# Kernel tuning notes

Hardware: AMD Instinct MI355X
Metric: run time of the kernel (lower is better)

The kernel has to match this reference:

```python
import jax, jax.numpy as jnp
import numpy as np

B = 16; L_IN = 512; D_MODEL = 512; N_HEAD = 8; D_K = 128; D_V = 128
D_FF = 2048; N_LAYER = 4; WINDOW = (4, 4, 4); INNER = 5; COV = 4; NUM_SEQ = 128
N_LVL = len(WINDOW) + 1


def _build_mask_sizes():
    # Pyraformer get_mask: intra-scale band + inter-scale parent/child links.
    all_size = [L_IN]
    for w in WINDOW:
        all_size.append(all_size[-1] // w)
    L = sum(all_size)
    vis = np.zeros((L, L), dtype=bool)
    iw = INNER // 2
    starts = [0]
    for s in all_size:
        starts.append(starts[-1] + s)
    for li, sz in enumerate(all_size):
        s = starts[li]
        for i in range(s, s + sz):
            vis[i, max(i - iw, s):min(i + iw + 1, s + sz)] = True
    for li in range(1, len(all_size)):
        s = starts[li]
        for i in range(s, s + all_size[li]):
            l = (s - all_size[li - 1]) + (i - s) * WINDOW[li - 1]
            if i == s + all_size[li] - 1:
                r = s
            else:
                r = (s - all_size[li - 1]) + (i - s + 1) * WINDOW[li - 1]
            vis[i, l:r] = True
            vis[l:r, i] = True
    return ~vis, all_size  # True = blocked


def _build_indexes(all_size):
    # Pyraformer refer_points: for each fine position, its ancestor at each scale.
    idx = np.zeros((L_IN, len(all_size)), dtype=np.int64)
    for i in range(L_IN):
        idx[i, 0] = i
        former = i
        for j in range(1, len(all_size)):
            start = sum(all_size[:j])
            inner = former - (start - all_size[j - 1])
            former = start + min(inner // WINDOW[j - 1], all_size[j] - 1)
            idx[i, j] = former
    return idx


def _layer_norm(x, g, b, eps=1e-5):
    m = x.mean(-1, keepdims=True)
    v = x.var(-1, keepdims=True)
    return (x - m) / jnp.sqrt(v + eps) * g + b


def _conv1d(x, w, stride):  # x: [B,C,L], w: [O,I,K]
    return jax.lax.conv_general_dilated(x, w, (stride,), 'VALID',
                                        dimension_numbers=('NCH', 'OIH', 'NCH'))


def _forward(x, cov_w, cov_b, data_conv_w, down_w, down_b, conv_w, conv_b, bn_g, bn_b,
             up_w, up_b, bln_g, bln_b, wq, wk, wv, fc_w, ln1_g, ln1_b,
             ffn_w1, ffn_b1, ffn_w2, ffn_b2, ln2_g, ln2_b, attn_mask, gather_idx):
    Bsz = x.shape[0]
    # SingleStepEmbedding
    covs = jnp.concatenate([x[:, :, 1:1 + COV], (x[:, :, -1] / NUM_SEQ - 0.5)[..., None]], -1)
    cov_emb = covs @ cov_w + cov_b
    data = x[:, :, 0][:, None, :]                      # [B,1,L]
    data = jnp.concatenate([data[:, :, -1:], data, data[:, :, :1]], -1)  # circular pad k=3
    data_emb = _conv1d(data, data_conv_w, 1).transpose(0, 2, 1)          # [B,L,D]
    i = jnp.arange(D_MODEL)
    vec = jnp.power(10000.0, 2.0 * (i // 2) / D_MODEL)
    ang = jnp.arange(L_IN)[:, None] / vec
    pos_emb = jnp.where(i % 2 == 0, jnp.sin(ang), jnp.cos(ang))
    seq = cov_emb + data_emb + pos_emb[None]
    # Bottleneck_Construct (down -> strided convs -> up -> concat -> LN)
    tmp = (seq @ down_w + down_b).transpose(0, 2, 1)   # [B,d_k,L]
    outs = []
    for s in range(len(WINDOW)):
        tmp = _conv1d(tmp, conv_w[s], WINDOW[s]) + conv_b[s][None, :, None]
        mu = tmp.mean((0, 2), keepdims=True)
        var = tmp.var((0, 2), keepdims=True)
        tmp = (tmp - mu) / jnp.sqrt(var + 1e-5) * bn_g[s][None, :, None] + bn_b[s][None, :, None]
        tmp = jax.nn.elu(tmp)
        outs.append(tmp)
    pyr = jnp.concatenate(outs, axis=2).transpose(0, 2, 1) @ up_w + up_b
    enc = _layer_norm(jnp.concatenate([seq, pyr], axis=1), bln_g, bln_b)  # [B,Ltot,D]
    Lt = enc.shape[1]
    scale = np.float32(1.0 / np.sqrt(D_K))
    for l in range(N_LAYER):
        q = (enc @ wq[l]).reshape(Bsz, Lt, N_HEAD, D_K).transpose(0, 2, 1, 3)
        k = (enc @ wk[l]).reshape(Bsz, Lt, N_HEAD, D_K).transpose(0, 2, 1, 3)
        v = (enc @ wv[l]).reshape(Bsz, Lt, N_HEAD, D_V).transpose(0, 2, 1, 3)
        scores = jnp.einsum('bhqd,bhkd->bhqk', q, k) * scale
        scores = jnp.where(attn_mask[None, None], -1e9, scores)
        attn = jax.nn.softmax(scores, -1)
        o = jnp.einsum('bhqk,bhkd->bhqd', attn, v).transpose(0, 2, 1, 3).reshape(Bsz, Lt, N_HEAD * D_V)
        enc = _layer_norm(o @ fc_w[l] + enc, ln1_g[l], ln1_b[l])  # post-norm
        h = jax.nn.gelu(enc @ ffn_w1[l] + ffn_b1[l], approximate=False) @ ffn_w2[l] + ffn_b2[l]
        enc = _layer_norm(enc + h, ln2_g[l], ln2_b[l])
    # refer_points gather: [B, L_IN, N_LVL*D]
    out = enc[:, gather_idx.reshape(-1), :].reshape(Bsz, L_IN, N_LVL * D_MODEL)
    return out


def setup_inputs() -> dict:
    key = jax.random.key(0)
    ks = iter(jax.random.split(key, 64))

    def nrm(shape, scale=0.02):
        return (jax.random.normal(next(ks), shape) * scale).astype(jnp.float32)

    covs = jax.random.normal(next(ks), (B, L_IN, COV + 1), jnp.float32)
    ids = jax.random.randint(next(ks), (B, L_IN), 0, NUM_SEQ).astype(jnp.float32)
    x = jnp.concatenate([covs, ids[..., None]], -1)  # col0=data, 1..COV=covs, last=series id
    mask_np, all_size = _build_mask_sizes()
    idx = _build_indexes(all_size)
    nw = len(WINDOW)
    return dict(
        x=x,
        cov_w=nrm((COV + 1, D_MODEL)), cov_b=jnp.zeros((D_MODEL,), jnp.float32),
        data_conv_w=nrm((D_MODEL, 1, 3)),
        down_w=nrm((D_MODEL, D_K)), down_b=jnp.zeros((D_K,), jnp.float32),
        conv_w=nrm((nw, D_K, D_K, WINDOW[0])), conv_b=jnp.zeros((nw, D_K), jnp.float32),
        bn_g=jnp.ones((nw, D_K), jnp.float32), bn_b=jnp.zeros((nw, D_K), jnp.float32),
        up_w=nrm((D_K, D_MODEL)), up_b=jnp.zeros((D_MODEL,), jnp.float32),
        bln_g=jnp.ones((D_MODEL,), jnp.float32), bln_b=jnp.zeros((D_MODEL,), jnp.float32),
        wq=nrm((N_LAYER, D_MODEL, N_HEAD * D_K)), wk=nrm((N_LAYER, D_MODEL, N_HEAD * D_K)),
        wv=nrm((N_LAYER, D_MODEL, N_HEAD * D_V)), fc_w=nrm((N_LAYER, N_HEAD * D_V, D_MODEL)),
        ln1_g=jnp.ones((N_LAYER, D_MODEL), jnp.float32), ln1_b=jnp.zeros((N_LAYER, D_MODEL), jnp.float32),
        ffn_w1=nrm((N_LAYER, D_MODEL, D_FF)), ffn_b1=jnp.zeros((N_LAYER, D_FF), jnp.float32),
        ffn_w2=nrm((N_LAYER, D_FF, D_MODEL)), ffn_b2=jnp.zeros((N_LAYER, D_MODEL), jnp.float32),
        ln2_g=jnp.ones((N_LAYER, D_MODEL), jnp.float32), ln2_b=jnp.zeros((N_LAYER, D_MODEL), jnp.float32),
        attn_mask=jnp.asarray(mask_np),
        gather_idx=jnp.asarray(idx),
    )


def reference(x, cov_w, cov_b, data_conv_w, down_w, down_b, conv_w, conv_b, bn_g, bn_b,
              up_w, up_b, bln_g, bln_b, wq, wk, wv, fc_w, ln1_g, ln1_b,
              ffn_w1, ffn_b1, ffn_w2, ffn_b2, ln2_g, ln2_b, attn_mask, gather_idx):
    return _forward(x, cov_w, cov_b, data_conv_w, down_w, down_b, conv_w, conv_b, bn_g, bn_b,
                    up_w, up_b, bln_g, bln_b, wq, wk, wv, fc_w, ln1_g, ln1_b,
                    ffn_w1, ffn_b1, ffn_w2, ffn_b2, ln2_g, ln2_b, attn_mask, gather_idx)
```

## Files before the change

### kernel.cpp

```cpp
#include <hip/hip_runtime.h>
#include <math.h>

typedef unsigned short u16;
typedef unsigned int u32;
typedef __attribute__((ext_vector_type(8))) short s16x8;
typedef __attribute__((ext_vector_type(4))) float f32x4;
typedef __attribute__((ext_vector_type(4))) u32 u32x4;
typedef __attribute__((ext_vector_type(2))) u32 u32x2;

#define LT 680

static __device__ __forceinline__ float bf2f(u16 u) {
  u32 v = ((u32)u) << 16;
  return __builtin_bit_cast(float, v);
}
static __device__ __forceinline__ u16 f2bf(float f) {
  u32 u = __builtin_bit_cast(u32, f);
  u32 r = (u + 0x7FFFu + ((u >> 16) & 1u)) >> 16;
  return (u16)r;
}
static __device__ __forceinline__ float lo16(u32 u) {
  return __builtin_bit_cast(float, u << 16);
}
static __device__ __forceinline__ float hi16(u32 u) {
  return __builtin_bit_cast(float, u & 0xFFFF0000u);
}

static __device__ __forceinline__ void gload16(const u16* g, u16* l) {
  __builtin_amdgcn_global_load_lds(
      (const __attribute__((address_space(1))) u32*)g,
      (__attribute__((address_space(3))) u32*)l, 16, 0, 0);
}

__global__ void detect_k(const u32* __restrict__ blng, int* __restrict__ flag) {
  if (threadIdx.x == 0 && blockIdx.x == 0)
    *flag = (blng[0] == 0x3F803F80u) ? 1 : 0;
}

struct CvtArgs {
  const void* src[20];
  float* dst[20];
  int pre[21];
};

__global__ __launch_bounds__(256) void cvtall_k(CvtArgs a, const int* __restrict__ flag) {
  int i = blockIdx.x * 256 + threadIdx.x;
  if (i >= a.pre[20]) return;
  int s = 0;
#pragma unroll
  for (int k = 1; k <= 20; ++k)
    if (i >= a.pre[k]) s = k;
  int j = i - a.pre[s];
  bool isb = (*flag != 0);
  a.dst[s][j] = isb ? bf2f(((const u16*)a.src[s])[j]) : ((const float*)a.src[s])[j];
}

__global__ __launch_bounds__(256) void tc2_k(const void* __restrict__ S,
                                             u16* __restrict__ D, int K, int N,
                                             size_t sstride, size_t dstride,
                                             const int* __restrict__ flag) {
  __shared__ u16 t[32][33];
  size_t soff = (size_t)blockIdx.z * sstride;
  D += (size_t)blockIdx.z * dstride;
  int nb = blockIdx.x * 32, kb = blockIdx.y * 32;
  int lx = threadIdx.x & 31, ly = threadIdx.x >> 5;
  bool isb = (*flag != 0);
#pragma unroll
  for (int i = 0; i < 4; ++i) {
    size_t idx = soff + (size_t)(kb + ly + 8 * i) * N + nb + lx;
    t[ly + 8 * i][lx] = isb ? ((const u16*)S)[idx] : f2bf(((const float*)S)[idx]);
  }
  __syncthreads();
#pragma unroll
  for (int i = 0; i < 4; ++i)
    D[(size_t)(nb + ly + 8 * i) * K + kb + lx] = t[lx][ly + 8 * i];
}

__global__ void cvb_k(const void* __restrict__ S, u16* __restrict__ D, int n,
                      const int* __restrict__ flag) {
  int i = blockIdx.x * 256 + threadIdx.x;
  if (i >= n) return;
  D[i] = (*flag) ? ((const u16*)S)[i] : f2bf(((const float*)S)[i]);
}

static __device__ __forceinline__ void reduce2_256(float& a, float& b, float* sm) {
#pragma unroll
  for (int o = 32; o; o >>= 1) { a += __shfl_xor(a, o); b += __shfl_xor(b, o); }
  int w = threadIdx.x >> 6, ln = threadIdx.x & 63;
  if (ln == 0) { sm[w] = a; sm[4 + w] = b; }
  __syncthreads();
  a = sm[0] + sm[1] + sm[2] + sm[3];
  b = sm[4] + sm[5] + sm[6] + sm[7];
  __syncthreads();
}

__global__ __launch_bounds__(256) void pos_k(float* __restrict__ post) {
  int l = blockIdx.x;
  int d0 = threadIdx.x << 1;
  float ex = (float)d0 * (1.0f / 512.0f);
  float vec = powf(10000.0f, ex);
  float ang = (float)l / vec;
  post[(l << 9) + d0] = sinf(ang);
  post[(l << 9) + d0 + 1] = cosf(ang);
}

__global__ __launch_bounds__(256) void emb_k(
    const float* __restrict__ x, const float* __restrict__ covw,
    const float* __restrict__ covb, const float* __restrict__ dw,
    const float* __restrict__ post, u16* __restrict__ seqb) {
  int r = blockIdx.x;
  int b = r >> 9, l = r & 511;
  int base = r * 6;
  float c0 = x[base + 1], c1 = x[base + 2];
  float c2 = x[base + 3], c3 = x[base + 4];
  float c4 = x[base + 5] * 0.0078125f - 0.5f;
  int lm = (l + 511) & 511, lp = (l + 1) & 511;
  float dm = x[((b << 9) + lm) * 6];
  float d0 = x[base];
  float dp = x[((b << 9) + lp) * 6];
  for (int d = threadIdx.x; d < 512; d += 256) {
    float cov = c0 * covw[d] + c1 * covw[512 + d] +
                c2 * covw[1024 + d] + c3 * covw[1536 + d] +
                c4 * covw[2048 + d] + covb[d];
    float cv = dm * dw[d * 3] + d0 * dw[d * 3 + 1] + dp * dw[d * 3 + 2];
    float v = cov + cv + post[(l << 9) + d];
    seqb[((size_t)r << 9) + d] = f2bf(v);
  }
}

static __device__ __forceinline__ f32x4 mfma16(s16x8 a, s16x8 b, f32x4 c) {
  return __builtin_amdgcn_mfma_f32_16x16x32_bf16(a, b, c, 0, 0, 0);
}

__global__ __launch_bounds__(256) void mgemm_k(
    const u16* __restrict__ A, const u16* __restrict__ BT,
    const float* __restrict__ bias, void* __restrict__ C,
    int M, int N, int K, int flags) {
  __shared__ char smem[49152];
  float* st = (float*)smem;
  int tid = threadIdx.x;

  int nN = N >> 7;
  int nwg = gridDim.x;
  int bid = blockIdx.x;
  int qq = nwg >> 3, rr = nwg & 7;
  int xcd = bid & 7, lin = bid >> 3;
  int s_ = (xcd < rr ? xcd * (qq + 1) : rr * (qq + 1) + (xcd - rr) * qq) + lin;
  int m0 = (s_ / nN) << 7, n0 = (s_ % nN) << 7;

  int l = tid & 63, wid = tid >> 6;
  int wr = wid >> 1, wc = wid & 1;
  f32x4 acc[4][4];
#pragma unroll
  for (int i = 0; i < 4; ++i)
#pragma unroll
    for (int j = 0; j < 4; ++j)
#pragma unroll
      for (int r = 0; r < 4; ++r) acc[i][j][r] = 0.f;

  int L8 = l >> 3;
  int p0_ = (l & 7) ^ L8;
  int rloc = 2 * L8 + (p0_ >> 2);
  int cel = (p0_ & 3) << 3;
  const u16* Ag0 = A + (size_t)m0 * K;
  const u16* Bg0 = BT + (size_t)n0 * K;

  auto STAGE = [&](int c, int kt) {
    u16* Ad = (u16*)smem + c * 8192;
    u16* Bd = Ad + 4096;
#pragma unroll
    for (int i = 0; i < 2; ++i) {
      int rg = wid * 32 + i * 16 + rloc;
      gload16(Ag0 + (size_t)rg * K + kt + cel, &Ad[(wid * 16 + i * 8) * 64]);
      gload16(Bg0 + (size_t)rg * K + kt + cel, &Bd[(wid * 16 + i * 8) * 64]);
    }
  };

  int sfrag = (((l & 1) << 2) + (l >> 4)) ^ (((l & 15) >> 1));
  int lhalf = (l & 15) >> 1;

  int nt = K >> 5;
  STAGE(0, 0);
  STAGE(1, 32);
  for (int t = 0; t < nt; ++t) {
    int cur = t % 3;
    if (t + 1 < nt) {
      asm volatile("s_waitcnt vmcnt(4)" ::: "memory");
    } else {
      asm volatile("s_waitcnt vmcnt(0)" ::: "memory");
    }
    __builtin_amdgcn_s_barrier();
    if (t + 2 < nt) STAGE((t + 2) % 3, (t + 2) << 5);
    const u16* Asb = (const u16*)smem + cur * 8192;
    const u16* Bsb = Asb + 4096;
    s16x8 af[4];
#pragma unroll
    for (int fr = 0; fr < 4; ++fr)
      af[fr] = *reinterpret_cast<const s16x8*>(
          &Asb[(wr * 32 + fr * 8 + lhalf) * 64 + sfrag * 8]);
#pragma unroll
    for (int fc = 0; fc < 4; ++fc) {
      s16x8 bf = *reinterpret_cast<const s16x8*>(
          &Bsb[(wc * 32 + fc * 8 + lhalf) * 64 + sfrag * 8]);
#pragma unroll
      for (int fr = 0; fr < 4; ++fr)
        acc[fr][fc] = mfma16(af[fr], bf, acc[fr][fc]);
    }
    asm volatile("s_waitcnt lgkmcnt(0)" ::: "memory");
  }
  __builtin_amdgcn_s_barrier();

  int cl = l & 15, rg2 = l >> 4;
  float bj[4];
#pragma unroll
  for (int fc = 0; fc < 4; ++fc)
    bj[fc] = bias ? bias[n0 + wc * 64 + fc * 16 + cl] : 0.f;
  int sr2 = tid >> 3;
  int scg = (tid & 7) << 4;
  int growb = m0 + ((sr2 >> 4) << 6) + (sr2 & 15);
#pragma unroll
  for (int fr = 0; fr < 4; ++fr) {
#pragma unroll
    for (int fc = 0; fc < 4; ++fc) {
      int col = wc * 64 + fc * 16 + cl;
#pragma unroll
      for (int r = 0; r < 4; ++r) {
        float v = acc[fr][fc][r] + bj[fc];
        if (flags & 2) {
          float zz = 1.5957691f * fmaf(0.044715f * v, v * v, v);
          v = v / (1.0f + __expf(-zz));
        }
        st[(wr * 16 + rg2 * 4 + r) * 132 + col] = v;
      }
    }
    __syncthreads();
    int gr = growb + fr * 16;
    if (flags & 1) {
      u32x4 o0, o1;
      u16* p0 = (u16*)&o0; u16* p1 = (u16*)&o1;
#pragma unroll
      for (int i = 0; i < 8; ++i) p0[i] = f2bf(st[sr2 * 132 + scg + i]);
#pragma unroll
      for (int i = 0; i < 8; ++i) p1[i] = f2bf(st[sr2 * 132 + scg + 8 + i]);
      u16* dst = (u16*)C + (size_t)gr * N + n0 + scg;
      __builtin_nontemporal_store(o0, reinterpret_cast<u32x4*>(dst));
      __builtin_nontemporal_store(o1, reinterpret_cast<u32x4*>(dst + 8));
    } else {
      float* dst = (float*)C + (size_t)gr * N + n0 + scg;
#pragma unroll
      for (int i = 0; i < 4; ++i)
        __builtin_nontemporal_store(
            *reinterpret_cast<const f32x4*>(&st[sr2 * 132 + scg + 4 * i]),
            reinterpret_cast<f32x4*>(dst + 4 * i));
    }
    __syncthreads();
  }
}

__global__ __launch_bounds__(256) void mg64_k(
    const u16* __restrict__ A, const u16* __restrict__ BT,
    const float* __restrict__ bias, u16* __restrict__ C,
    int M, int N, int K) {
  __shared__ char smem[49152];
  float* st = (float*)smem;
  int tid = threadIdx.x;

  int nN = N >> 6;
  int nwg = gridDim.x;
  int bid = blockIdx.x;
  int qq = nwg >> 3, rr = nwg & 7;
  int xcd = bid & 7, lin = bid >> 3;
  int s_ = (xcd < rr ? xcd * (qq + 1) : rr * (qq + 1) + (xcd - rr) * qq) + lin;
  int m0 = (s_ / nN) << 6, n0 = (s_ % nN) << 6;

  int l = tid & 63, wid = tid >> 6;
  f32x4 acc[4];
#pragma unroll
  for (int j = 0; j < 4; ++j)
#pragma unroll
    for (int r = 0; r < 4; ++r) acc[j][r] = 0.f;

  int row8 = l >> 3, cp = l & 7;
  int cg = (cp ^ (row8 & 7)) << 3;
  const u16* Ag0 = A + (size_t)m0 * K;
  const u16* Bg0 = BT + (size_t)n0 * K;

  auto STAGE = [&](int c, int kt) {
    u16* Ad = (u16*)smem + c * 8192;
    u16* Bd = Ad + 4096;
#pragma unroll
    for (int i = 0; i < 2; ++i) {
      int r = wid * 16 + i * 8 + row8;
      gload16(Ag0 + (size_t)r * K + kt + cg, &Ad[(wid * 16 + i * 8) * 64]);
      gload16(Bg0 + (size_t)r * K + kt + cg, &Bd[(wid * 16 + i * 8) * 64]);
    }
  };

  int nt = K >> 6;
  STAGE(0, 0);
  STAGE(1, 64);
  for (int t = 0; t < nt; ++t) {
    int cur = t % 3;
    if (t + 1 < nt) {
      asm volatile("s_waitcnt vmcnt(4)" ::: "memory");
    } else {
      asm volatile("s_waitcnt vmcnt(0)" ::: "memory");
    }
    __builtin_amdgcn_s_barrier();
    if (t + 2 < nt) STAGE((t + 2) % 3, (t + 2) << 6);
    const u16* Asb = (const u16*)smem + cur * 8192;
    const u16* Bsb = Asb + 4096;
#pragma unroll
    for (int kk = 0; kk < 2; ++kk) {
      int kc = ((kk * 4 + (l >> 4)) ^ (l & 7)) * 8;
      s16x8 af = *reinterpret_cast<const s16x8*>(
          &Asb[(wid * 16 + (l & 15)) * 64 + kc]);
#pragma unroll
      for (int fc = 0; fc < 4; ++fc) {
        s16x8 bf = *reinterpret_cast<const s16x8*>(
            &Bsb[(fc * 16 + (l & 15)) * 64 + kc]);
        acc[fc] = mfma16(af, bf, acc[fc]);
      }
    }
    asm volatile("s_waitcnt lgkmcnt(0)" ::: "memory");
  }
  __builtin_amdgcn_s_barrier();

  int cl = l & 15, rg = l >> 4;
  float bj[4];
#pragma unroll
  for (int fc = 0; fc < 4; ++fc)
    bj[fc] = bias ? bias[n0 + fc * 16 + cl] : 0.f;
#pragma unroll
  for (int fc = 0; fc < 4; ++fc)
#pragma unroll
    for (int r = 0; r < 4; ++r)
      st[(wid * 16 + rg * 4 + r) * 80 + fc * 16 + cl] = acc[fc][r] + bj[fc];
  __syncthreads();
  int rr2 = tid >> 3;
  int cc2 = (tid & 7) << 3;
#pragma unroll
  for (int ps = 0; ps < 2; ++ps) {
    int row = rr2 + ps * 32;
    u32x4 o;
    u16* pp = (u16*)&o;
#pragma unroll
    for (int i = 0; i < 8; ++i) pp[i] = f2bf(st[row * 80 + cc2 + i]);
    __builtin_nontemporal_store(
        o, reinterpret_cast<u32x4*>(C + (size_t)(m0 + row) * N + n0 + cc2));
  }
}

__global__ void im2colb_k(const float* __restrict__ Y, u16* __restrict__ X,
                          int Ti, int To) {
  int e = blockIdx.x * 256 + threadIdx.x;
  int ik = e & 511;
  int bt = e >> 9;
  int b = bt / To, t = bt - b * To;
  int i = ik >> 2, k = ik & 3;
  X[e] = f2bf(Y[((size_t)(b * Ti + (t << 2) + k) << 7) + i]);
}

__global__ __launch_bounds__(256) void bnelu_k(float* __restrict__ Y,
                                               const float* __restrict__ g,
                                               const float* __restrict__ be, int Ms) {
  __shared__ float sm[8];
  int ch = blockIdx.x;
  float s = 0.f, s2 = 0.f;
  for (int i = threadIdx.x; i < Ms; i += 256) {
    float v = Y[((size_t)i << 7) + ch];
    s += v; s2 += v * v;
  }
  reduce2_256(s, s2, sm);
  float mu = s / (float)Ms;
  float var = s2 / (float)Ms - mu * mu;
  float inv = rsqrtf(var + 1e-5f);
  float ga = g[ch], bb = be[ch];
  for (int i = threadIdx.x; i < Ms; i += 256) {
    float v = (Y[((size_t)i << 7) + ch] - mu) * inv * ga + bb;
    Y[((size_t)i << 7) + ch] = (v > 0.f) ? v : (expf(v) - 1.0f);
  }
}

__global__ void scat_k(const float* __restrict__ Y, u16* __restrict__ catb,
                       int Ts, int off) {
  int e = blockIdx.x * 256 + threadIdx.x;
  int i = e & 127;
  int bt = e >> 7;
  int b = bt / Ts, t = bt - b * Ts;
  catb[((size_t)(b * 168 + off + t) << 7) + i] = f2bf(Y[e]);
}

__global__ __launch_bounds__(256) void catln_k(
    const u16* __restrict__ seqb, const u16* __restrict__ pyrb,
    const float* __restrict__ g, const float* __restrict__ be,
    u16* __restrict__ outb) {
  __shared__ float sm[8];
  int row = blockIdx.x;
  int b = row / LT, j = row - b * LT;
  const u16* src = (j < 512) ? (seqb + ((size_t)(b * 512 + j) << 9))
                             : (pyrb + ((size_t)(b * 168 + j - 512) << 9));
  int t = threadIdx.x;
  float x0 = bf2f(src[t]), x1 = bf2f(src[t + 256]);
  float s = x0 + x1, s2 = x0 * x0 + x1 * x1;
  reduce2_256(s, s2, sm);
  float mu = s * 0.001953125f;
  float var = s2 * 0.001953125f - mu * mu;
  float inv = rsqrtf(var + 1e-5f);
  size_t ob = (size_t)row << 9;
  outb[ob + t] = f2bf((x0 - mu) * inv * g[t] + be[t]);
  outb[ob + t + 256] = f2bf((x1 - mu) * inv * g[t + 256] + be[t + 256]);
}

__global__ __launch_bounds__(256) void lnres_k(
    const u16* __restrict__ A, u16* R,
    const float* __restrict__ g, const float* __restrict__ be) {
  __shared__ float sm[8];
  int row = blockIdx.x;
  size_t base = (size_t)row << 9;
  int t = threadIdx.x;
  float x0 = bf2f(A[base + t]) + bf2f(R[base + t]);
  float x1 = bf2f(A[base + t + 256]) + bf2f(R[base + t + 256]);
  float s = x0 + x1, s2 = x0 * x0 + x1 * x1;
  reduce2_256(s, s2, sm);
  float mu = s * 0.001953125f;
  float var = s2 * 0.001953125f - mu * mu;
  float inv = rsqrtf(var + 1e-5f);
  R[base + t] = f2bf((x0 - mu) * inv * g[t] + be[t]);
  R[base + t + 256] = f2bf((x1 - mu) * inv * g[t + 256] + be[t + 256]);
}

__global__ __launch_bounds__(256) void attn_k(const u16* __restrict__ QKV,
                                              u16* __restrict__ O) {
  int cpx = gridDim.x >> 3;
  int bq = (blockIdx.x & 7) * cpx + (blockIdx.x >> 3);
  int b = bq / LT, q = bq - b * LT;
  int lane = threadIdx.x & 63, wv = threadIdx.x >> 6;
  int half = lane >> 5, t4 = (lane & 31) << 2;
  int h = (wv << 1) + half;
  int lvl = (q < 512) ? 0 : (q < 640) ? 1 : (q < 672) ? 2 : 3;
  int Sl = (lvl == 0) ? 0 : (lvl == 1) ? 512 : (lvl == 2) ? 640 : 672;
  int SZl = (lvl == 0) ? 512 : (lvl == 1) ? 128 : (lvl == 2) ? 32 : 8;
  int p = q - Sl;
  int Sc = (lvl == 1) ? 0 : (lvl == 2) ? 512 : 640;
  int Sp = (lvl == 0) ? 512 : (lvl == 1) ? 640 : 672;
  int tg[10];
  bool vd[10];
#pragma unroll
  for (int jj = 0; jj < 10; ++jj) {
    int tgt; bool valid;
    if (jj < 5) { int pp = p - 2 + jj; valid = (pp >= 0 && pp < SZl); tgt = Sl + pp; }
    else if (jj < 9) { valid = (lvl > 0); tgt = Sc + p * 4 + (jj - 5); }
    else { valid = (lvl < 3); tgt = Sp + (p >> 2); }
    if (!valid) tgt = q;
    tg[jj] = tgt; vd[jj] = valid;
  }
  size_t hoff = h * 128 + t4;
  u32x2 qv = *reinterpret_cast<const u32x2*>(QKV + (size_t)bq * 3072 + hoff);
  float q0 = lo16(qv.x), q1 = hi16(qv.x), q2 = lo16(qv.y), q3 = hi16(qv.y);
  size_t base3 = (size_t)b * LT;
  float sc[10];
  float mx = -1e30f;
#pragma unroll
  for (int jj = 0; jj < 10; ++jj) {
    u32x2 kv = *reinterpret_cast<const u32x2*>(
        QKV + (base3 + tg[jj]) * 3072 + 1024 + hoff);
    float pr = q0 * lo16(kv.x) + q1 * hi16(kv.x) + q2 * lo16(kv.y) + q3 * hi16(kv.y);
#pragma unroll
    for (int o = 16; o; o >>= 1) pr += __shfl_xor(pr, o);
    float sv = vd[jj] ? pr * 0.08838834764831845f : -1e30f;
    sc[jj] = sv;
    mx = fmaxf(mx, sv);
  }
  float den = 0.f;
#pragma unroll
  for (int jj = 0; jj < 10; ++jj) { sc[jj] = expf(sc[jj] - mx); den += sc[jj]; }
  float invd = 1.0f / den;
  float o0 = 0.f, o1 = 0.f, o2 = 0.f, o3 = 0.f;
#pragma unroll
  for (int jj = 0; jj < 10; ++jj) {
    u32x2 vv = *reinterpret_cast<const u32x2*>(
        QKV + (base3 + tg[jj]) * 3072 + 2048 + hoff);
    float w = sc[jj] * invd;
    o0 = fmaf(w, lo16(vv.x), o0);
    o1 = fmaf(w, hi16(vv.x), o1);
    o2 = fmaf(w, lo16(vv.y), o2);
    o3 = fmaf(w, hi16(vv.y), o3);
  }
  u32x2 ov;
  ov.x = (u32)f2bf(o0) | ((u32)f2bf(o1) << 16);
  ov.y = (u32)f2bf(o2) | ((u32)f2bf(o3) << 16);
  *reinterpret_cast<u32x2*>(O + (size_t)bq * 1024 + hoff) = ov;
}

__global__ void gather_k(const u16* __restrict__ encb, void* __restrict__ out,
                         const int* __restrict__ flag) {
  int e = blockIdx.x * 256 + threadIdx.x;
  int d = e & 511;
  int lvl = (e >> 9) & 3;
  int i = (e >> 11) & 511;
  int b = e >> 20;
  int g = (lvl == 0) ? i
        : (lvl == 1) ? (512 + (i >> 2))
        : (lvl == 2) ? (640 + (i >> 4))
                     : (672 + (i >> 6));
  u16 v = encb[(((size_t)b * LT + g) << 9) + d];
  if (*flag) ((u16*)out)[e] = v;
  else       ((float*)out)[e] = bf2f(v);
}

extern "C" void kernel_launch(void* const* d_in, const int* in_sizes, int n_in,
                              void* d_out, int out_size, void* d_ws, size_t ws_size,
                              hipStream_t stream) {
  float* ws = (float*)d_ws;
  size_t off = 0;
  auto alloc = [&](size_t n) { float* p = ws + off; off += (n + 63) & ~(size_t)63; return p; };

  int* flag = (int*)alloc(64);

  static const int cvt_n[26] = {
      49152, 2560, 512, 1536, 65536, 128, 196608, 384, 384, 384,
      65536, 512, 512, 512, 2097152, 2097152, 2097152, 2097152, 2048, 2048,
      4194304, 8192, 4194304, 2048, 2048, 2048};
  float* cf[26];
  for (int i = 0; i < 26; ++i) {
    if (i == 4 || i == 6 || i == 10 || i == 14 || i == 15 || i == 16 ||
        i == 17 || i == 20 || i == 22) {
      cf[i] = nullptr;
      continue;
    }
    cf[i] = alloc(cvt_n[i]);
  }

  float* post    = alloc((size_t)512 * 512);
  u16*   tmp     = (u16*)alloc((size_t)10880 * 512 / 2);
  u16*   encb    = (u16*)alloc((size_t)10880 * 512 / 2);
  u16*   qkv     = (u16*)alloc((size_t)10880 * 3072 / 2);
  u16*   attnout = (u16*)alloc((size_t)10880 * 1024 / 2);
  u16*   qkvw    = (u16*)alloc((size_t)4 * 3072 * 512 / 2);
  u16*   fcT     = (u16*)alloc((size_t)4 * 512 * 1024 / 2);
  u16*   w1T     = (u16*)alloc((size_t)4 * 2048 * 512 / 2);
  u16*   w2T     = (u16*)alloc((size_t)4 * 512 * 2048 / 2);
  u16*   dwT     = (u16*)alloc((size_t)128 * 512 / 2);
  u16*   upT     = (u16*)alloc((size_t)512 * 128 / 2);
  u16*   cwb     = (u16*)alloc((size_t)3 * 128 * 512 / 2);
  u16*   seqb    = (u16*)alloc((size_t)8192 * 512 / 2);
  u16*   pyrb    = (u16*)alloc((size_t)2688 * 512 / 2);
  float* tdown   = alloc((size_t)8192 * 128);
  float* ya      = alloc((size_t)2048 * 128);
  float* yb      = alloc((size_t)512 * 128);
  float* yc      = alloc((size_t)128 * 128);
  u16*   catb    = (u16*)alloc((size_t)2688 * 128 / 2);
  u16*   xcolb   = (u16*)alloc((size_t)2048 * 512 / 2);
  u16*   H1      = qkv;

  detect_k<<<1, 64, 0, stream>>>((const u32*)d_in[12], flag);
  {
    static const int segs[17] = {0,1,2,3,5,7,8,9,11,12,13,18,19,21,23,24,25};
    CvtArgs a;
    int acc_ = 0;
    for (int k = 0; k < 17; ++k) {
      int i = segs[k];
      a.src[k] = d_in[i];
      a.dst[k] = cf[i];
      a.pre[k] = acc_;
      acc_ += cvt_n[i];
    }
    for (int k = 17; k <= 20; ++k) {
      a.pre[k] = acc_;
      if (k < 20) { a.src[k] = d_in[0]; a.dst[k] = cf[0]; }
    }
    cvtall_k<<<(acc_ + 255) / 256, 256, 0, stream>>>(a, flag);
  }

  const float *x = cf[0], *covw = cf[1], *covb = cf[2], *dconvw = cf[3],
              *downb = cf[5], *convb = cf[7],
              *bng = cf[8], *bnb = cf[9], *upb = cf[11],
              *blng = cf[12], *blnb = cf[13], *ln1g = cf[18], *ln1b = cf[19],
              *b1 = cf[21], *b2 = cf[23], *ln2g = cf[24], *ln2b = cf[25];

  tc2_k<<<dim3(32, 16, 4), 256, 0, stream>>>(d_in[14], qkvw,           512, 1024, 524288, 1572864, flag);
  tc2_k<<<dim3(32, 16, 4), 256, 0, stream>>>(d_in[15], qkvw + 524288,  512, 1024, 524288, 1572864, flag);
  tc2_k<<<dim3(32, 16, 4), 256, 0, stream>>>(d_in[16], qkvw + 1048576, 512, 1024, 524288, 1572864, flag);
  tc2_k<<<dim3(16, 32, 4), 256, 0, stream>>>(d_in[17], fcT,  1024, 512, 524288, 524288, flag);
  tc2_k<<<dim3(64, 16, 4), 256, 0, stream>>>(d_in[20], w1T,  512, 2048, 1048576, 1048576, flag);
  tc2_k<<<dim3(16, 64, 4), 256, 0, stream>>>(d_in[22], w2T,  2048, 512, 1048576, 1048576, flag);
  tc2_k<<<dim3(4, 16, 1), 256, 0, stream>>>(d_in[4],  dwT, 512, 128, 0, 0, flag);
  tc2_k<<<dim3(16, 4, 1), 256, 0, stream>>>(d_in[10], upT, 128, 512, 0, 0, flag);
  cvb_k<<<(196608 + 255) / 256, 256, 0, stream>>>(d_in[6], cwb, 196608, flag);

  pos_k<<<512, 256, 0, stream>>>(post);
  emb_k<<<8192, 256, 0, stream>>>(x, covw, covb, dconvw, post, seqb);

  mgemm_k<<<64, 256, 0, stream>>>(seqb, dwT, downb, tdown, 8192, 128, 512, 0);
  im2colb_k<<<(16 * 128 * 512) / 256, 256, 0, stream>>>(tdown, xcolb, 512, 128);
  mgemm_k<<<16, 256, 0, stream>>>(xcolb, cwb, convb, ya, 2048, 128, 512, 0);
  bnelu_k<<<128, 256, 0, stream>>>(ya, bng, bnb, 2048);
  scat_k<<<(2048 * 128) / 256, 256, 0, stream>>>(ya, catb, 128, 0);
  im2colb_k<<<(16 * 32 * 512) / 256, 256, 0, stream>>>(ya, xcolb, 128, 32);
  mgemm_k<<<4, 256, 0, stream>>>(xcolb, cwb + 65536, convb + 128, yb, 512, 128, 512, 0);
  bnelu_k<<<128, 256, 0, stream>>>(yb, bng + 128, bnb + 128, 512);
  scat_k<<<(512 * 128) / 256, 256, 0, stream>>>(yb, catb, 32, 128);
  im2colb_k<<<(16 * 8 * 512) / 256, 256, 0, stream>>>(yb, xcolb, 32, 8);
  mgemm_k<<<1, 256, 0, stream>>>(xcolb, cwb + 131072, convb + 256, yc, 128, 128, 512, 0);
  bnelu_k<<<128, 256, 0, stream>>>(yc, bng + 256, bnb + 256, 128);
  scat_k<<<(128 * 128) / 256, 256, 0, stream>>>(yc, catb, 8, 160);
  mgemm_k<<<21 * 4, 256, 0, stream>>>(catb, upT, upb, pyrb, 2688, 512, 128, 1);
  catln_k<<<10880, 256, 0, stream>>>(seqb, pyrb, blng, blnb, encb);

  for (int l = 0; l < 4; ++l) {
    const u16* qw  = qkvw + (size_t)l * 3072 * 512;
    const u16* fw  = fcT + (size_t)l * 524288;
    const u16* w1w = w1T + (size_t)l * 1048576;
    const u16* w2w = w2T + (size_t)l * 1048576;
    mgemm_k<<<85 * 24, 256, 0, stream>>>(encb, qw, nullptr, qkv, 10880, 3072, 512, 1);
    attn_k<<<16 * LT, 256, 0, stream>>>(qkv, attnout);
    mg64_k<<<170 * 8, 256, 0, stream>>>(attnout, fw, nullptr, tmp, 10880, 512, 1024);
    lnres_k<<<10880, 256, 0, stream>>>(tmp, encb, ln1g + l * 512, ln1b + l * 512);
    mgemm_k<<<85 * 16, 256, 0, stream>>>(encb, w1w, b1 + l * 2048, H1, 10880, 2048, 512, 3);
    mg64_k<<<170 * 8, 256, 0, stream>>>(H1, w2w, b2 + l * 512, tmp, 10880, 512, 2048);
    lnres_k<<<10880, 256, 0, stream>>>(tmp, encb, ln2g + l * 512, ln2b + l * 512);
  }

  gather_k<<<(16 * 512 * 2048) / 256, 256, 0, stream>>>(encb, d_out, flag);
}
```

Before: 1.088 ms.

## Widen N=512 GEMM tile to 128x64 with per-wave private LDS staging

Replaces the 64x64 GEMM used for the fc and FFN-down projections with a 128x64 tile in which each wave stages its own 32-row A slice and a full copy of the 64-column B slice in a private LDS region. The k-step drops to 32, the pipeline becomes double-buffered, and the per-iteration block barrier is removed. The aim is more MFMA work per B fragment and less block-level synchronisation. In exchange, B is loaded redundantly by all four waves, the grid is halved to 680 blocks, which may reduce occupancy across CUs, and the shorter k-step means more loop iterations.

```diff
diff --git a/kernel.cpp b/kernel.cpp
--- a/kernel.cpp
+++ b/kernel.cpp
@@ -257,7 +257,7 @@
   }
 }
 
-__global__ __launch_bounds__(256) void mg64_k(
+__global__ __launch_bounds__(256) void mg64w_k(
     const u16* __restrict__ A, const u16* __restrict__ BT,
     const float* __restrict__ bias, u16* __restrict__ C,
     int M, int N, int K) {
@@ -271,60 +271,67 @@
   int qq = nwg >> 3, rr = nwg & 7;
   int xcd = bid & 7, lin = bid >> 3;
   int s_ = (xcd < rr ? xcd * (qq + 1) : rr * (qq + 1) + (xcd - rr) * qq) + lin;
-  int m0 = (s_ / nN) << 6, n0 = (s_ % nN) << 6;
+  int m0 = (s_ / nN) << 7, n0 = (s_ % nN) << 6;
 
   int l = tid & 63, wid = tid >> 6;
-  f32x4 acc[4];
-#pragma unroll
-  for (int j = 0; j < 4; ++j)
-#pragma unroll
-    for (int r = 0; r < 4; ++r) acc[j][r] = 0.f;
-
-  int row8 = l >> 3, cp = l & 7;
-  int cg = (cp ^ (row8 & 7)) << 3;
-  const u16* Ag0 = A + (size_t)m0 * K;
+  f32x4 acc[2][4];
+#pragma unroll
+  for (int i = 0; i < 2; ++i)
+#pragma unroll
+    for (int j = 0; j < 4; ++j)
+#pragma unroll
+      for (int r = 0; r < 4; ++r) acc[i][j][r] = 0.f;
+
+  int L8 = l >> 3;
+  int p0_ = (l & 7) ^ L8;
+  int rloc = 2 * L8 + (p0_ >> 2);
+  int cel = (p0_ & 3) << 3;
+  const u16* Ag0 = A + (size_t)(m0 + wid * 32) * K;
   const u16* Bg0 = BT + (size_t)n0 * K;
+  u16* wbase = (u16*)smem + wid * 6144;
 
   auto STAGE = [&](int c, int kt) {
-    u16* Ad = (u16*)smem + c * 8192;
-    u16* Bd = Ad + 4096;
-#pragma unroll
-    for (int i = 0; i < 2; ++i) {
-      int r = wid * 16 + i * 8 + row8;
-      gload16(Ag0 + (size_t)r * K + kt + cg, &Ad[(wid * 16 + i * 8) * 64]);
-      gload16(Bg0 + (size_t)r * K + kt + cg, &Bd[(wid * 16 + i * 8) * 64]);
-    }
+    u16* Ad = wbase + c * 3072;
+    u16* Bd = Ad + 1024;
+#pragma unroll
+    for (int i = 0; i < 2; ++i)
+      gload16(Ag0 + (size_t)(i * 16 + rloc) * K + kt + cel, &Ad[i * 512]);
+#pragma unroll
+    for (int i = 0; i < 4; ++i)
+      gload16(Bg0 + (size_t)(i * 16 + rloc) * K + kt + cel, &Bd[i * 512]);
   };
 
-  int nt = K >> 6;
+  int sfrag = (((l & 1) << 2) + (l >> 4)) ^ (((l & 15) >> 1));
+  int lhalf = (l & 15) >> 1;
+
+  int nt = K >> 5;
   STAGE(0, 0);
-  STAGE(1, 64);
   for (int t = 0; t < nt; ++t) {
-    int cur = t % 3;
+    int cur = t & 1;
     if (t + 1 < nt) {
-      asm volatile("s_waitcnt vmcnt(4)" ::: "memory");
+      STAGE(cur ^ 1, (t + 1) << 5);
+      asm volatile("s_waitcnt vmcnt(6)" ::: "memory");
     } else {
       asm volatile("s_waitcnt vmcnt(0)" ::: "memory");
     }
-    __builtin_amdgcn_s_barrier();
-    if (t + 2 < nt) STAGE((t + 2) % 3, (t + 2) << 6);
-    const u16* Asb = (const u16*)smem + cur * 8192;
-    const u16* Bsb = Asb + 4096;
-#pragma unroll
-    for (int kk = 0; kk < 2; ++kk) {
-      int kc = ((kk * 4 + (l >> 4)) ^ (l & 7)) * 8;
-      s16x8 af = *reinterpret_cast<const s16x8*>(
-          &Asb[(wid * 16 + (l & 15)) * 64 + kc]);
-#pragma unroll
-      for (int fc = 0; fc < 4; ++fc) {
-        s16x8 bf = *reinterpret_cast<const s16x8*>(
-            &Bsb[(fc * 16 + (l & 15)) * 64 + kc]);
-        acc[fc] = mfma16(af, bf, acc[fc]);
-      }
+    const u16* Ad = wbase + cur * 3072;
+    const u16* Bd = Ad + 1024;
+    s16x8 af[2];
+#pragma unroll
+    for (int fr = 0; fr < 2; ++fr)
+      af[fr] = *reinterpret_cast<const s16x8*>(
+          &Ad[(fr * 8 + lhalf) * 64 + sfrag * 8]);
+#pragma unroll
+    for (int fc = 0; fc < 4; ++fc) {
+      s16x8 bf = *reinterpret_cast<const s16x8*>(
+          &Bd[(fc * 8 + lhalf) * 64 + sfrag * 8]);
+#pragma unroll
+      for (int fr = 0; fr < 2; ++fr)
+        acc[fr][fc] = mfma16(af[fr], bf, acc[fr][fc]);
     }
     asm volatile("s_waitcnt lgkmcnt(0)" ::: "memory");
   }
-  __builtin_amdgcn_s_barrier();
+  __syncthreads();
 
   int cl = l & 15, rg = l >> 4;
   float bj[4];
@@ -332,15 +339,18 @@
   for (int fc = 0; fc < 4; ++fc)
     bj[fc] = bias ? bias[n0 + fc * 16 + cl] : 0.f;
 #pragma unroll
-  for (int fc = 0; fc < 4; ++fc)
-#pragma unroll
-    for (int r = 0; r < 4; ++r)
-      st[(wid * 16 + rg * 4 + r) * 80 + fc * 16 + cl] = acc[fc][r] + bj[fc];
+  for (int fr = 0; fr < 2; ++fr)
+#pragma unroll
+    for (int fc = 0; fc < 4; ++fc)
+#pragma unroll
+      for (int r = 0; r < 4; ++r)
+        st[(wid * 32 + fr * 16 + rg * 4 + r) * 80 + fc * 16 + cl] =
+            acc[fr][fc][r] + bj[fc];
   __syncthreads();
   int rr2 = tid >> 3;
   int cc2 = (tid & 7) << 3;
 #pragma unroll
-  for (int ps = 0; ps < 2; ++ps) {
+  for (int ps = 0; ps < 4; ++ps) {
     int row = rr2 + ps * 32;
     u32x4 o;
     u16* pp = (u16*)&o;
@@ -615,10 +625,10 @@
     const u16* w2w = w2T + (size_t)l * 1048576;
     mgemm_k<<<85 * 24, 256, 0, stream>>>(encb, qw, nullptr, qkv, 10880, 3072, 512, 1);
     attn_k<<<16 * LT, 256, 0, stream>>>(qkv, attnout);
-    mg64_k<<<170 * 8, 256, 0, stream>>>(attnout, fw, nullptr, tmp, 10880, 512, 1024);
+    mg64w_k<<<85 * 8, 256, 0, stream>>>(attnout, fw, nullptr, tmp, 10880, 512, 1024);
     lnres_k<<<10880, 256, 0, stream>>>(tmp, encb, ln1g + l * 512, ln1b + l * 512);
     mgemm_k<<<85 * 16, 256, 0, stream>>>(encb, w1w, b1 + l * 2048, H1, 10880, 2048, 512, 3);
-    mg64_k<<<170 * 8, 256, 0, stream>>>(H1, w2w, b2 + l * 512, tmp, 10880, 512, 2048);
+    mg64w_k<<<85 * 8, 256, 0, stream>>>(H1, w2w, b2 + l * 512, tmp, 10880, 512, 2048);
     lnres_k<<<10880, 256, 0, stream>>>(tmp, encb, ln2g + l * 512, ln2b + l * 512);
   }
 
```

New measurement: 1.172 ms. 7.8% more time.
